# Optimization experiments

Measured on AMD Instinct MI355X. Metric: run time of the kernel, lower is better.

Reference implementation:

```python
import jax, jax.numpy as jnp
import numpy as np

N_HEAD = 8
DQK = 64
DV = 64
D_IN = 512
D_OUT = 512
D_MID = 2048
B = 4
L = 2048
EPS = 1e-5


def layernorm(x):
    mu = jnp.mean(x, axis=-1, keepdims=True)
    var = jnp.mean(jnp.square(x - mu), axis=-1, keepdims=True)
    return (x - mu) / jnp.sqrt(var + EPS)


def setup_inputs() -> dict:
    key = jax.random.key(0)
    ks = jax.random.split(key, 10)
    s = 0.02
    return {
        "query": jax.random.normal(ks[0], (B, L, D_IN), jnp.float32),
        "key": jax.random.normal(ks[1], (B, L, D_IN), jnp.float32),
        "value": jax.random.normal(ks[2], (B, L, D_IN), jnp.float32),
        "mask": jnp.zeros((B, L, L), jnp.float32),
        "WQ": jax.random.normal(ks[3], (D_IN, N_HEAD * DQK), jnp.float32) * s,
        "WK": jax.random.normal(ks[4], (D_IN, N_HEAD * DQK), jnp.float32) * s,
        "WV": jax.random.normal(ks[5], (D_IN, N_HEAD * DV), jnp.float32) * s,
        "WO": jax.random.normal(ks[6], (N_HEAD * DV, D_OUT), jnp.float32) * s,
        "W1": jax.random.normal(ks[7], (D_OUT, D_MID), jnp.float32) * s,
        "W2": jax.random.normal(ks[8], (D_MID, D_OUT), jnp.float32) * s,
    }


def reference(query, key, value, mask, WQ, WK, WV, WO, W1, W2):
    bsz = query.shape[0]
    # projections -> [b, h, l, d]
    Q = (query @ WQ).reshape(bsz, -1, N_HEAD, DQK).transpose(0, 2, 1, 3)
    K = (key @ WK).reshape(bsz, -1, N_HEAD, DQK).transpose(0, 2, 1, 3)
    V = (value @ WV).reshape(bsz, -1, N_HEAD, DV).transpose(0, 2, 1, 3)
    # scaled dot-product attention with additive mask [b, 1, lq, lk]
    scores = jnp.einsum("bhqd,bhkd->bhqk", Q, K) / jnp.sqrt(jnp.float32(DQK))
    w = jax.nn.softmax(scores + mask[:, None, :, :], axis=-1)
    out = jnp.einsum("bhqk,bhkd->bhqd", w, V)
    out = out.transpose(0, 2, 1, 3).reshape(bsz, -1, N_HEAD * DV)
    out = out @ WO
    out = layernorm(query + out)
    ff = jax.nn.relu(out @ W1) @ W2
    return layernorm(out + ff)
```

## Files before the change

kernel.cpp:

```cpp
#include <hip/hip_runtime.h>
#include <hip/hip_bf16.h>

using bf16 = __bf16;
typedef __bf16 bf16x4 __attribute__((ext_vector_type(4)));
typedef __bf16 bf16x8 __attribute__((ext_vector_type(8)));
typedef float f32x4 __attribute__((ext_vector_type(4)));
typedef float f32x16 __attribute__((ext_vector_type(16)));
typedef unsigned uint2v __attribute__((ext_vector_type(2)));

static constexpr int BATCH = 4;
static constexpr int SEQ   = 2048;
static constexpr int DIN   = 512;
static constexpr int NHEAD = 8;
static constexpr int DMID  = 2048;
static constexpr int MROWS = BATCH * SEQ;

__device__ __forceinline__ void gload16(const void* g, void* l)
{
    __builtin_amdgcn_global_load_lds(
        (const __attribute__((address_space(1))) unsigned int*)g,
        (__attribute__((address_space(3))) unsigned int*)l, 16, 0, 0);
}

__device__ __forceinline__ unsigned cvtpk(float a, float b)
{
    unsigned r;
    asm("v_cvt_pk_bf16_f32 %0, %1, %2" : "=v"(r) : "v"(a), "v"(b));
    return r;
}

__device__ __forceinline__ float fexp2(float x)
{
    float r;
    asm("v_exp_f32 %0, %1" : "=v"(r) : "v"(x));
    return r;
}

__global__ __launch_bounds__(256) void tw_mask(
    const float* __restrict__ WQ, const float* __restrict__ WK,
    const float* __restrict__ WV, const float* __restrict__ WO,
    const float* __restrict__ W1, const float* __restrict__ W2,
    bf16* __restrict__ WQt, bf16* __restrict__ WKt, bf16* __restrict__ WVt,
    bf16* __restrict__ WOt, bf16* __restrict__ W1t, bf16* __restrict__ W2t,
    const float* __restrict__ q, const float* __restrict__ k,
    const float* __restrict__ v,
    bf16* __restrict__ qb, bf16* __restrict__ kb, bf16* __restrict__ vb,
    const uint4* __restrict__ mask, int* __restrict__ flag)
{
    const int bid = blockIdx.x;
    if (bid >= 4096) {
        const int idx = bid - 4096;
        const float* src = idx < 1024 ? q : idx < 2048 ? k : v;
        bf16*       dst = idx < 1024 ? qb : idx < 2048 ? kb : vb;
        const size_t b4 = (size_t)(idx & 1023) * 1024;
#pragma unroll
        for (int i = 0; i < 4; ++i) {
            const float4 f = reinterpret_cast<const float4*>(src)[b4 + i * 256 + threadIdx.x];
            bf16x4 h;
            h[0] = (bf16)f.x; h[1] = (bf16)f.y; h[2] = (bf16)f.z; h[3] = (bf16)f.w;
            reinterpret_cast<bf16x4*>(dst)[b4 + i * 256 + threadIdx.x] = h;
        }
        return;
    }
    if (bid >= 3072) {
        const uint4* p = mask + (size_t)(bid - 3072) * 4096;
        unsigned nz = 0;
#pragma unroll
        for (int i = 0; i < 16; ++i) {
            const uint4 u = p[i * 256 + threadIdx.x];
            nz |= u.x | u.y | u.z | u.w;
        }
        if (nz) atomicOr(flag, 1);
        return;
    }
    __shared__ float tile[32][33];
    const float* in; bf16* out; int ip, op, cx, ry;
    if (bid < 1024) {
        const int w = bid >> 8, idx = bid & 255;
        in  = w == 0 ? WQ  : w == 1 ? WK  : w == 2 ? WV  : WO;
        out = w == 0 ? WQt : w == 1 ? WKt : w == 2 ? WVt : WOt;
        ip = 512; op = 512; cx = idx & 15; ry = idx >> 4;
    } else if (bid < 2048) {
        const int idx = bid - 1024;
        in = W1; out = W1t; ip = 2048; op = 512; cx = idx & 63; ry = idx >> 6;
    } else {
        const int idx = bid - 2048;
        in = W2; out = W2t; ip = 512; op = 2048; cx = idx & 15; ry = idx >> 4;
    }
    const int c0 = cx * 32, r0 = ry * 32;
    const int tx = threadIdx.x & 31, ty = threadIdx.x >> 5;
    for (int i = 0; i < 32; i += 8)
        tile[ty + i][tx] = in[(size_t)(r0 + ty + i) * ip + c0 + tx];
    __syncthreads();
    for (int i = 0; i < 32; i += 8)
        out[(size_t)(c0 + ty + i) * op + r0 + tx] = (bf16)tile[tx][ty + i];
}

template <int ACT>
__global__ __launch_bounds__(256) void gemm128(const bf16* __restrict__ A,
                                               const bf16* __restrict__ Bt,
                                               bf16* __restrict__ C,
                                               int N, int K)
{
    __shared__ bf16 sA[128 * 64];
    __shared__ bf16 sB[128 * 64];

    const int t    = threadIdx.x;
    const int lane = t & 63;
    const int wave = t >> 6;
    const int wm   = wave >> 1;
    const int wn   = wave & 1;
    const int lr   = lane & 15;
    const int lq   = lane >> 4;

    const int m0 = blockIdx.y * 128;
    const int n0 = blockIdx.x * 128;

    const int srow = lane >> 3;
    const int scol = (lane & 7) * 8;

    f32x4 acc[4][4] = {};

    for (int k0 = 0; k0 < K; k0 += 64) {
        if (k0) __syncthreads();
#pragma unroll
        for (int i = 0; i < 4; ++i) {
            const int ch = wave * 4 + i;
            const int r  = ch * 8 + srow;
            gload16(A  + (size_t)(m0 + r) * K + k0 + scol, sA + ch * 512);
            gload16(Bt + (size_t)(n0 + r) * K + k0 + scol, sB + ch * 512);
        }
        __syncthreads();

#pragma unroll
        for (int kk = 0; kk < 2; ++kk) {
            bf16x8 af[4], bfr[4];
#pragma unroll
            for (int x = 0; x < 4; ++x) {
                af[x]  = *reinterpret_cast<const bf16x8*>(&sA[(wm * 64 + x * 16 + lr) * 64 + kk * 32 + lq * 8]);
                bfr[x] = *reinterpret_cast<const bf16x8*>(&sB[(wn * 64 + x * 16 + lr) * 64 + kk * 32 + lq * 8]);
            }
#pragma unroll
            for (int m = 0; m < 4; ++m)
#pragma unroll
                for (int n = 0; n < 4; ++n)
                    acc[m][n] = __builtin_amdgcn_mfma_f32_16x16x32_bf16(af[m], bfr[n], acc[m][n], 0, 0, 0);
        }
    }

#pragma unroll
    for (int n = 0; n < 4; ++n) {
        const int col = n0 + wn * 64 + n * 16 + lr;
#pragma unroll
        for (int m = 0; m < 4; ++m) {
            const int rowb = m0 + wm * 64 + m * 16 + lq * 4;
#pragma unroll
            for (int j = 0; j < 4; ++j) {
                float v = acc[m][n][j];
                if (ACT == 1) v = v > 0.f ? v : 0.f;
                C[(size_t)(rowb + j) * N + col] = (bf16)v;
            }
        }
    }
}

__global__ __launch_bounds__(256) void gemm64_qkvb(const bf16* __restrict__ qb,
                                                   const bf16* __restrict__ kb,
                                                   const bf16* __restrict__ vb,
                                                   const bf16* __restrict__ WQt,
                                                   const bf16* __restrict__ WKt,
                                                   const bf16* __restrict__ WVt,
                                                   bf16* __restrict__ Qb,
                                                   bf16* __restrict__ Kb,
                                                   bf16* __restrict__ Vt)
{
    __shared__ bf16 sA[64 * 64];
    __shared__ bf16 sB[128 * 64];

    const bf16* A  = blockIdx.z == 0 ? qb  : blockIdx.z == 1 ? kb  : vb;
    const bf16* Bt = blockIdx.z == 0 ? WQt : blockIdx.z == 1 ? WKt : WVt;
    const int K = DIN;

    const int t    = threadIdx.x;
    const int lane = t & 63;
    const int wave = t >> 6;
    const int lr   = lane & 15;
    const int lq   = lane >> 4;

    const int m0 = blockIdx.y * 64;
    const int n0 = blockIdx.x * 128;

    const int srow = lane >> 3;
    const int scol = (lane & 7) * 8;

    f32x4 acc[4][2] = {};

    for (int k0 = 0; k0 < K; k0 += 64) {
        if (k0) __syncthreads();
#pragma unroll
        for (int i = 0; i < 2; ++i) {
            const int ch = wave * 2 + i;
            gload16(A + (size_t)(m0 + ch * 8 + srow) * K + k0 + scol, sA + ch * 512);
        }
#pragma unroll
        for (int i = 0; i < 4; ++i) {
            const int ch = wave * 4 + i;
            gload16(Bt + (size_t)(n0 + ch * 8 + srow) * K + k0 + scol, sB + ch * 512);
        }
        __syncthreads();

#pragma unroll
        for (int kk = 0; kk < 2; ++kk) {
            bf16x8 af[4], bfr[2];
#pragma unroll
            for (int x = 0; x < 4; ++x)
                af[x] = *reinterpret_cast<const bf16x8*>(&sA[(x * 16 + lr) * 64 + kk * 32 + lq * 8]);
#pragma unroll
            for (int n = 0; n < 2; ++n)
                bfr[n] = *reinterpret_cast<const bf16x8*>(&sB[(wave * 32 + n * 16 + lr) * 64 + kk * 32 + lq * 8]);
#pragma unroll
            for (int m = 0; m < 4; ++m)
#pragma unroll
                for (int n = 0; n < 2; ++n)
                    acc[m][n] = __builtin_amdgcn_mfma_f32_16x16x32_bf16(af[m], bfr[n], acc[m][n], 0, 0, 0);
        }
    }

    if (blockIdx.z < 2) {
        bf16* C = blockIdx.z == 0 ? Qb : Kb;
#pragma unroll
        for (int n = 0; n < 2; ++n) {
            const int col = n0 + wave * 32 + n * 16 + lr;
#pragma unroll
            for (int m = 0; m < 4; ++m) {
                const int rowb = m0 + m * 16 + lq * 4;
#pragma unroll
                for (int j = 0; j < 4; ++j)
                    C[(size_t)(rowb + j) * DIN + col] = (bf16)acc[m][n][j];
            }
        }
    } else {
        __syncthreads();
#pragma unroll
        for (int n = 0; n < 2; ++n)
#pragma unroll
            for (int m = 0; m < 4; ++m)
#pragma unroll
                for (int j = 0; j < 4; ++j)
                    sB[(wave * 32 + n * 16 + lr) * 64 + m * 16 + lq * 4 + j] = (bf16)acc[m][n][j];
        __syncthreads();
        const int c = t >> 1, half = t & 1;
#pragma unroll
        for (int qq = 0; qq < 4; ++qq) {
            const bf16x8 vv = *reinterpret_cast<const bf16x8*>(&sB[c * 64 + half * 32 + qq * 8]);
            *reinterpret_cast<bf16x8*>(Vt + (size_t)(n0 + c) * MROWS + m0 + half * 32 + qq * 8) = vv;
        }
    }
}

__global__ __launch_bounds__(256) void attn_kernel(const bf16* __restrict__ Qb,
                                                   const bf16* __restrict__ Kb,
                                                   const bf16* __restrict__ Vt,
                                                   const float* __restrict__ mask,
                                                   bf16* __restrict__ O,
                                                   const int* __restrict__ mzf)
{
    const int bi   = blockIdx.x;
    const int xcd  = bi & 7;
    const int slot = bi >> 3;
    const int pair = xcd * 4 + (slot >> 3);
    const int qt   = slot & 7;
    const int h    = pair >> 2;
    const int b    = pair & 3;

    const int t    = threadIdx.x;
    const int lane = t & 63;
    const int wave = t >> 6;
    const int l31  = lane & 31;
    const int hi   = lane >> 5;
    const int q0   = qt * 256;
    const bool useM = (*mzf != 0);

    __shared__ bf16 sK[64 * 64];
    __shared__ bf16 sV[64 * 64];
    __shared__ float sL[4][64];

    bf16x8 qf[2][4];
#pragma unroll
    for (int g = 0; g < 2; ++g)
#pragma unroll
        for (int s = 0; s < 4; ++s)
            qf[g][s] = *reinterpret_cast<const bf16x8*>(
                Qb + (size_t)(b * SEQ + q0 + wave * 64 + g * 32 + l31) * DIN + h * 64 + s * 16 + hi * 8);

    f32x16 o[2][2] = {};
    float lacc[2] = {};

    const int sr = t >> 2;
    const int c1 = t & 3;

    const bf16* kbase = Kb + (size_t)(b * SEQ) * DIN + h * 64;
    const bf16* vbase = Vt + (size_t)(h * 64 + sr) * MROWS + b * SEQ;

    constexpr float L2E = 1.4426950408889634f;
    constexpr float SCL = 0.125f * L2E;

    int4 kr0 = *reinterpret_cast<const int4*>(kbase + (size_t)sr * DIN + c1 * 8);
    int4 kr1 = *reinterpret_cast<const int4*>(kbase + (size_t)sr * DIN + c1 * 8 + 32);
    int4 vr0 = *reinterpret_cast<const int4*>(vbase + c1 * 8);
    int4 vr1 = *reinterpret_cast<const int4*>(vbase + c1 * 8 + 32);

    for (int tile = 0; tile < SEQ / 64; ++tile) {
        if (tile) __syncthreads();

        {
            const int x = sr & 7;
            *reinterpret_cast<int4*>(&sK[sr * 64 + ((c1    ) ^ x) * 8]) = kr0;
            *reinterpret_cast<int4*>(&sK[sr * 64 + ((c1 + 4) ^ x) * 8]) = kr1;
            *reinterpret_cast<int4*>(&sV[sr * 64 + ((c1    ) ^ x) * 8]) = vr0;
            *reinterpret_cast<int4*>(&sV[sr * 64 + ((c1 + 4) ^ x) * 8]) = vr1;
        }

        if (tile + 1 < SEQ / 64) {
            const int k0 = (tile + 1) * 64;
            kr0 = *reinterpret_cast<const int4*>(kbase + (size_t)(k0 + sr) * DIN + c1 * 8);
            kr1 = *reinterpret_cast<const int4*>(kbase + (size_t)(k0 + sr) * DIN + c1 * 8 + 32);
            vr0 = *reinterpret_cast<const int4*>(vbase + k0 + c1 * 8);
            vr1 = *reinterpret_cast<const int4*>(vbase + k0 + c1 * 8 + 32);
        }
        __syncthreads();

        bf16x8 kf[2][4];
#pragma unroll
        for (int kb = 0; kb < 2; ++kb)
#pragma unroll
            for (int s = 0; s < 4; ++s) {
                const int r = kb * 32 + l31;
                kf[kb][s] = *reinterpret_cast<const bf16x8*>(
                    &sK[r * 64 + ((hi + 2 * s) ^ (r & 7)) * 8]);
            }
        bf16x8 vf[2][4];
#pragma unroll
        for (int dt = 0; dt < 2; ++dt)
#pragma unroll
            for (int c = 0; c < 4; ++c) {
                const int r = dt * 32 + l31;
                vf[dt][c] = *reinterpret_cast<const bf16x8*>(
                    &sV[r * 64 + ((hi + 2 * c) ^ (r & 7)) * 8]);
            }

#pragma unroll
        for (int g = 0; g < 2; ++g) {
            f32x16 st0 = {}, st1 = {};
#pragma unroll
            for (int s = 0; s < 4; ++s) {
                st0 = __builtin_amdgcn_mfma_f32_32x32x16_bf16(kf[0][s], qf[g][s], st0, 0, 0, 0);
                st1 = __builtin_amdgcn_mfma_f32_32x32x16_bf16(kf[1][s], qf[g][s], st1, 0, 0, 0);
            }

            float p[32];
            if (useM) {
                const float* mrow = mask + ((size_t)(b * SEQ + q0 + wave * 64 + g * 32 + l31)) * SEQ + tile * 64;
#pragma unroll
                for (int r = 0; r < 16; ++r) {
                    const int kk = (r & 3) + 8 * (r >> 2) + 4 * hi;
                    p[r]      = fexp2(fmaf(st0[r], SCL, mrow[kk]      * L2E));
                    p[16 + r] = fexp2(fmaf(st1[r], SCL, mrow[32 + kk] * L2E));
                }
            } else {
#pragma unroll
                for (int r = 0; r < 16; ++r) {
                    p[r]      = fexp2(st0[r] * SCL);
                    p[16 + r] = fexp2(st1[r] * SCL);
                }
            }
            {
                float s0 = 0.f, s1 = 0.f, s2 = 0.f, s3 = 0.f;
#pragma unroll
                for (int r = 0; r < 8; ++r) {
                    s0 += p[r];
                    s1 += p[8 + r];
                    s2 += p[16 + r];
                    s3 += p[24 + r];
                }
                lacc[g] += (s0 + s1) + (s2 + s3);
            }

            bf16x8 pa[4];
#pragma unroll
            for (int c = 0; c < 4; ++c) {
                const int bse = c * 8;
                unsigned u0 = cvtpk(p[bse + 0], p[bse + 1]);
                unsigned u1 = cvtpk(p[bse + 2], p[bse + 3]);
                unsigned u2 = cvtpk(p[bse + 4], p[bse + 5]);
                unsigned u3 = cvtpk(p[bse + 6], p[bse + 7]);
                const uint2v r02 = __builtin_amdgcn_permlane32_swap(u0, u2, false, false);
                const uint2v r13 = __builtin_amdgcn_permlane32_swap(u1, u3, false, false);
                union { unsigned u[4]; bf16x8 v; } pk;
                pk.u[0] = r02.x; pk.u[1] = r13.x; pk.u[2] = r02.y; pk.u[3] = r13.y;
                pa[c] = pk.v;
            }

#pragma unroll
            for (int c = 0; c < 4; ++c) {
                o[g][0] = __builtin_amdgcn_mfma_f32_32x32x16_bf16(pa[c], vf[0][c], o[g][0], 0, 0, 0);
                o[g][1] = __builtin_amdgcn_mfma_f32_32x32x16_bf16(pa[c], vf[1][c], o[g][1], 0, 0, 0);
            }
        }
    }

#pragma unroll
    for (int g = 0; g < 2; ++g)
        lacc[g] += __shfl_xor(lacc[g], 32);
    if (hi == 0) {
        sL[wave][l31]      = lacc[0];
        sL[wave][32 + l31] = lacc[1];
    }

#pragma unroll
    for (int g = 0; g < 2; ++g)
#pragma unroll
        for (int r = 0; r < 16; ++r) {
            const int qr = (r & 3) + 8 * (r >> 2) + 4 * hi;
            const float inv = 1.f / sL[wave][g * 32 + qr];
            const size_t rowoff = (size_t)(b * SEQ + q0 + wave * 64 + g * 32 + qr) * DIN + h * 64;
            O[rowoff + l31]      = (bf16)(o[g][0][r] * inv);
            O[rowoff + 32 + l31] = (bf16)(o[g][1][r] * inv);
        }
}

__global__ __launch_bounds__(512) void gemm_ln(const bf16* __restrict__ A,
                                               const bf16* __restrict__ Bt,
                                               const float* __restrict__ X,
                                               bf16* __restrict__ Onb,
                                               float* __restrict__ Onf,
                                               int K)
{
    __shared__ bf16 sA[2][32 * 64];
    __shared__ bf16 sB[2][512 * 64];
    __shared__ float sRed[32][8];
    __shared__ float sMu[32];
    __shared__ float sRstd[32];

    const int t    = threadIdx.x;
    const int lane = t & 63;
    const int w    = t >> 6;
    const int lr   = lane & 15;
    const int lq   = lane >> 4;
    const int srow = lane >> 3;
    const int scol = (lane & 7) * 8;

    const int m0 = blockIdx.x * 32;

    auto stage = [&](int s, int b) {
        const int k0 = s * 64;
#pragma unroll
        for (int i = 0; i < 8; ++i) {
            const int ch = w * 8 + i;
            gload16(Bt + (size_t)(ch * 8 + srow) * K + k0 + scol, &sB[b][ch * 512]);
        }
        if (w < 4)
            gload16(A + (size_t)(m0 + w * 8 + srow) * K + k0 + scol, &sA[b][w * 512]);
    };

    f32x4 acc[2][4] = {};
    const int steps = K / 64;

    stage(0, 0);
    __syncthreads();

    for (int s = 0; s < steps; ++s) {
        const int b = s & 1;
        if (s + 1 < steps) stage(s + 1, b ^ 1);

#pragma unroll
        for (int kk = 0; kk < 2; ++kk) {
            bf16x8 af[2], bfr[4];
#pragma unroll
            for (int m = 0; m < 2; ++m)
                af[m] = *reinterpret_cast<const bf16x8*>(&sA[b][(m * 16 + lr) * 64 + kk * 32 + lq * 8]);
#pragma unroll
            for (int n = 0; n < 4; ++n)
                bfr[n] = *reinterpret_cast<const bf16x8*>(&sB[b][(w * 64 + n * 16 + lr) * 64 + kk * 32 + lq * 8]);
#pragma unroll
            for (int m = 0; m < 2; ++m)
#pragma unroll
                for (int n = 0; n < 4; ++n)
                    acc[m][n] = __builtin_amdgcn_mfma_f32_16x16x32_bf16(af[m], bfr[n], acc[m][n], 0, 0, 0);
        }
        __syncthreads();
    }

#pragma unroll
    for (int m = 0; m < 2; ++m)
#pragma unroll
        for (int n = 0; n < 4; ++n)
#pragma unroll
            for (int j = 0; j < 4; ++j)
                acc[m][n][j] += X[(size_t)(m0 + m * 16 + lq * 4 + j) * DIN + w * 64 + n * 16 + lr];

#pragma unroll
    for (int m = 0; m < 2; ++m)
#pragma unroll
        for (int j = 0; j < 4; ++j) {
            float s = acc[m][0][j] + acc[m][1][j] + acc[m][2][j] + acc[m][3][j];
            s += __shfl_xor(s, 1); s += __shfl_xor(s, 2);
            s += __shfl_xor(s, 4); s += __shfl_xor(s, 8);
            if (lr == 0) sRed[m * 16 + lq * 4 + j][w] = s;
        }
    __syncthreads();
    if (t < 32) {
        float s = 0.f;
#pragma unroll
        for (int ww = 0; ww < 8; ++ww) s += sRed[t][ww];
        sMu[t] = s * (1.f / DIN);
    }
    __syncthreads();

#pragma unroll
    for (int m = 0; m < 2; ++m)
#pragma unroll
        for (int j = 0; j < 4; ++j) {
            const float mu = sMu[m * 16 + lq * 4 + j];
            float s = 0.f;
#pragma unroll
            for (int n = 0; n < 4; ++n) {
                const float d = acc[m][n][j] - mu;
                s += d * d;
            }
            s += __shfl_xor(s, 1); s += __shfl_xor(s, 2);
            s += __shfl_xor(s, 4); s += __shfl_xor(s, 8);
            if (lr == 0) sRed[m * 16 + lq * 4 + j][w] = s;
        }
    __syncthreads();
    if (t < 32) {
        float s = 0.f;
#pragma unroll
        for (int ww = 0; ww < 8; ++ww) s += sRed[t][ww];
        sRstd[t] = rsqrtf(s * (1.f / DIN) + 1e-5f);
    }
    __syncthreads();

#pragma unroll
    for (int m = 0; m < 2; ++m)
#pragma unroll
        for (int j = 0; j < 4; ++j) {
            const int rl = m * 16 + lq * 4 + j;
            const float mu = sMu[rl], rstd = sRstd[rl];
            const size_t rowoff = (size_t)(m0 + rl) * DIN;
#pragma unroll
            for (int n = 0; n < 4; ++n) {
                const float r = (acc[m][n][j] - mu) * rstd;
                const int col = w * 64 + n * 16 + lr;
                if (Onb) Onb[rowoff + col] = (bf16)r;
                if (Onf) Onf[rowoff + col] = r;
            }
        }
}

extern "C" void kernel_launch(void* const* d_in, const int* in_sizes, int n_in,
                              void* d_out, int out_size, void* d_ws, size_t ws_size,
                              hipStream_t stream)
{
    const float* query = (const float*)d_in[0];
    const float* key   = (const float*)d_in[1];
    const float* value = (const float*)d_in[2];
    const float* mask  = (const float*)d_in[3];
    const float* WQ    = (const float*)d_in[4];
    const float* WK    = (const float*)d_in[5];
    const float* WV    = (const float*)d_in[6];
    const float* WO    = (const float*)d_in[7];
    const float* W1    = (const float*)d_in[8];
    const float* W2    = (const float*)d_in[9];

    char* w = (char*)d_ws;
    size_t off = 0;
    auto carve2 = [&](size_t elems) { bf16* p = (bf16*)(w + off); off += elems * 2; return p; };
    auto carve4 = [&](size_t elems) { float* p = (float*)(w + off); off += elems * 4; return p; };

    bf16* Qb    = carve2((size_t)MROWS * DIN);
    bf16* Kb    = carve2((size_t)MROWS * DIN);
    bf16* Vb    = carve2((size_t)MROWS * DIN);
    bf16* Vt    = carve2((size_t)MROWS * DIN);
    bf16* Mid   = carve2((size_t)MROWS * DMID);
    float* Ln1f = carve4((size_t)MROWS * DIN);
    bf16* WQt   = carve2((size_t)DIN * DIN);
    bf16* WKt   = carve2((size_t)DIN * DIN);
    bf16* WVt   = carve2((size_t)DIN * DIN);
    bf16* WOt   = carve2((size_t)DIN * DIN);
    bf16* W1t   = carve2((size_t)DIN * DMID);
    bf16* W2t   = carve2((size_t)DMID * DIN);
    int*  mzf   = (int*)(w + off); off += 16;
    if (off > ws_size) return;

    bf16* Ob   = Vb;
    bf16* Ln1b = Kb;
    bf16* qb = Mid;
    bf16* kb = Mid + (size_t)MROWS * DIN;
    bf16* vb = Mid + (size_t)2 * MROWS * DIN;

    const dim3 blk(256);

    hipMemsetAsync(mzf, 0, 4, stream);

    tw_mask<<<dim3(7168), blk, 0, stream>>>(WQ, WK, WV, WO, W1, W2,
                                            WQt, WKt, WVt, WOt, W1t, W2t,
                                            query, key, value, qb, kb, vb,
                                            (const uint4*)mask, mzf);

    gemm64_qkvb<<<dim3(DIN / 128, MROWS / 64, 3), blk, 0, stream>>>(qb, kb, vb,
                                                                    WQt, WKt, WVt, Qb, Kb, Vt);

    attn_kernel<<<dim3(256), blk, 0, stream>>>(Qb, Kb, Vt, mask, Ob, mzf);

    gemm_ln<<<dim3(MROWS / 32), dim3(512), 0, stream>>>(Ob, WOt, query, Ln1b, Ln1f, DIN);

    gemm128<1><<<dim3(DMID / 128, MROWS / 128), blk, 0, stream>>>(Ln1b, W1t, Mid, DMID, DIN);

    gemm_ln<<<dim3(MROWS / 32), dim3(512), 0, stream>>>(Mid, W2t, Ln1f,
                                                        (bf16*)nullptr, (float*)d_out, DMID);
}
```

Measured before the change: 350.3 us.

## Double-buffer K/V tiles in attention and fold softmax scale into Q

The attention kernel now uses two LDS buffers for K and V. Each iteration stores the prefetched registers for tile+1 into the other buffer and issues global loads for tile+2, which leaves one barrier per tile instead of two. Separately, the QKV projection multiplies Q by 0.125*log2(e) before the bf16 store, so the per-element scale multiply disappears from the exp2 path. The cost is double the K/V shared memory and slightly different rounding, since the scaled Q is quantised to bf16.

```diff
diff --git a/kernel.cpp b/kernel.cpp
--- a/kernel.cpp
+++ b/kernel.cpp
@@ -14,6 +14,8 @@
 static constexpr int NHEAD = 8;
 static constexpr int DMID  = 2048;
 static constexpr int MROWS = BATCH * SEQ;
+
+static constexpr float QSCL = 0.125f * 1.4426950408889634f;
 
 __device__ __forceinline__ void gload16(const void* g, void* l)
 {
@@ -228,6 +230,7 @@
 
     if (blockIdx.z < 2) {
         bf16* C = blockIdx.z == 0 ? Qb : Kb;
+        const float sc = blockIdx.z == 0 ? QSCL : 1.f;
 #pragma unroll
         for (int n = 0; n < 2; ++n) {
             const int col = n0 + wave * 32 + n * 16 + lr;
@@ -236,7 +239,7 @@
                 const int rowb = m0 + m * 16 + lq * 4;
 #pragma unroll
                 for (int j = 0; j < 4; ++j)
-                    C[(size_t)(rowb + j) * DIN + col] = (bf16)acc[m][n][j];
+                    C[(size_t)(rowb + j) * DIN + col] = (bf16)(acc[m][n][j] * sc);
             }
         }
     } else {
@@ -281,8 +284,8 @@
     const int q0   = qt * 256;
     const bool useM = (*mzf != 0);
 
-    __shared__ bf16 sK[64 * 64];
-    __shared__ bf16 sV[64 * 64];
+    __shared__ bf16 sK[2][64 * 64];
+    __shared__ bf16 sV[2][64 * 64];
     __shared__ float sL[4][64];
 
     bf16x8 qf[2][4];
@@ -296,39 +299,46 @@
     f32x16 o[2][2] = {};
     float lacc[2] = {};
 
-    const int sr = t >> 2;
-    const int c1 = t & 3;
+    const int sr  = t >> 2;
+    const int c1  = t & 3;
+    const int xsw = sr & 7;
 
     const bf16* kbase = Kb + (size_t)(b * SEQ) * DIN + h * 64;
     const bf16* vbase = Vt + (size_t)(h * 64 + sr) * MROWS + b * SEQ;
 
     constexpr float L2E = 1.4426950408889634f;
-    constexpr float SCL = 0.125f * L2E;
 
     int4 kr0 = *reinterpret_cast<const int4*>(kbase + (size_t)sr * DIN + c1 * 8);
     int4 kr1 = *reinterpret_cast<const int4*>(kbase + (size_t)sr * DIN + c1 * 8 + 32);
     int4 vr0 = *reinterpret_cast<const int4*>(vbase + c1 * 8);
     int4 vr1 = *reinterpret_cast<const int4*>(vbase + c1 * 8 + 32);
+    *reinterpret_cast<int4*>(&sK[0][sr * 64 + ((c1    ) ^ xsw) * 8]) = kr0;
+    *reinterpret_cast<int4*>(&sK[0][sr * 64 + ((c1 + 4) ^ xsw) * 8]) = kr1;
+    *reinterpret_cast<int4*>(&sV[0][sr * 64 + ((c1    ) ^ xsw) * 8]) = vr0;
+    *reinterpret_cast<int4*>(&sV[0][sr * 64 + ((c1 + 4) ^ xsw) * 8]) = vr1;
+    kr0 = *reinterpret_cast<const int4*>(kbase + (size_t)(64 + sr) * DIN + c1 * 8);
+    kr1 = *reinterpret_cast<const int4*>(kbase + (size_t)(64 + sr) * DIN + c1 * 8 + 32);
+    vr0 = *reinterpret_cast<const int4*>(vbase + 64 + c1 * 8);
+    vr1 = *reinterpret_cast<const int4*>(vbase + 64 + c1 * 8 + 32);
+    __syncthreads();
 
     for (int tile = 0; tile < SEQ / 64; ++tile) {
-        if (tile) __syncthreads();
-
-        {
-            const int x = sr & 7;
-            *reinterpret_cast<int4*>(&sK[sr * 64 + ((c1    ) ^ x) * 8]) = kr0;
-            *reinterpret_cast<int4*>(&sK[sr * 64 + ((c1 + 4) ^ x) * 8]) = kr1;
-            *reinterpret_cast<int4*>(&sV[sr * 64 + ((c1    ) ^ x) * 8]) = vr0;
-            *reinterpret_cast<int4*>(&sV[sr * 64 + ((c1 + 4) ^ x) * 8]) = vr1;
-        }
+        const int cur = tile & 1;
 
         if (tile + 1 < SEQ / 64) {
-            const int k0 = (tile + 1) * 64;
+            const int nxt = cur ^ 1;
+            *reinterpret_cast<int4*>(&sK[nxt][sr * 64 + ((c1    ) ^ xsw) * 8]) = kr0;
+            *reinterpret_cast<int4*>(&sK[nxt][sr * 64 + ((c1 + 4) ^ xsw) * 8]) = kr1;
+            *reinterpret_cast<int4*>(&sV[nxt][sr * 64 + ((c1    ) ^ xsw) * 8]) = vr0;
+            *reinterpret_cast<int4*>(&sV[nxt][sr * 64 + ((c1 + 4) ^ xsw) * 8]) = vr1;
+        }
+        if (tile + 2 < SEQ / 64) {
+            const int k0 = (tile + 2) * 64;
             kr0 = *reinterpret_cast<const int4*>(kbase + (size_t)(k0 + sr) * DIN + c1 * 8);
             kr1 = *reinterpret_cast<const int4*>(kbase + (size_t)(k0 + sr) * DIN + c1 * 8 + 32);
             vr0 = *reinterpret_cast<const int4*>(vbase + k0 + c1 * 8);
             vr1 = *reinterpret_cast<const int4*>(vbase + k0 + c1 * 8 + 32);
         }
-        __syncthreads();
 
         bf16x8 kf[2][4];
 #pragma unroll
@@ -337,7 +347,7 @@
             for (int s = 0; s < 4; ++s) {
                 const int r = kb * 32 + l31;
                 kf[kb][s] = *reinterpret_cast<const bf16x8*>(
-                    &sK[r * 64 + ((hi + 2 * s) ^ (r & 7)) * 8]);
+                    &sK[cur][r * 64 + ((hi + 2 * s) ^ (r & 7)) * 8]);
             }
         bf16x8 vf[2][4];
 #pragma unroll
@@ -346,7 +356,7 @@
             for (int c = 0; c < 4; ++c) {
                 const int r = dt * 32 + l31;
                 vf[dt][c] = *reinterpret_cast<const bf16x8*>(
-                    &sV[r * 64 + ((hi + 2 * c) ^ (r & 7)) * 8]);
+                    &sV[cur][r * 64 + ((hi + 2 * c) ^ (r & 7)) * 8]);
             }
 
 #pragma unroll
@@ -364,14 +374,14 @@
 #pragma unroll
                 for (int r = 0; r < 16; ++r) {
                     const int kk = (r & 3) + 8 * (r >> 2) + 4 * hi;
-                    p[r]      = fexp2(fmaf(st0[r], SCL, mrow[kk]      * L2E));
-                    p[16 + r] = fexp2(fmaf(st1[r], SCL, mrow[32 + kk] * L2E));
+                    p[r]      = fexp2(st0[r] + mrow[kk]      * L2E);
+                    p[16 + r] = fexp2(st1[r] + mrow[32 + kk] * L2E);
                 }
             } else {
 #pragma unroll
                 for (int r = 0; r < 16; ++r) {
-                    p[r]      = fexp2(st0[r] * SCL);
-                    p[16 + r] = fexp2(st1[r] * SCL);
+                    p[r]      = fexp2(st0[r]);
+                    p[16 + r] = fexp2(st1[r]);
                 }
             }
             {
@@ -407,6 +417,8 @@
                 o[g][1] = __builtin_amdgcn_mfma_f32_32x32x16_bf16(pa[c], vf[1][c], o[g][1], 0, 0, 0);
             }
         }
+
+        __syncthreads();
     }
 
 #pragma unroll
```

Measured after the change: 352.9 us. No clear change (+0.7%).
